# Performance work log

Hardware: AMD Instinct MI355X
Metric: run time of the kernel (lower is better)

The kernel has to match this reference:

```python
import jax, jax.numpy as jnp
import numpy as np

DIM = 1024
NUM_HEADS = 16
HEAD_DIM = DIM // NUM_HEADS
SCALE = HEAD_DIM ** -0.5


def setup_inputs() -> dict:
    key = jax.random.key(0)
    k_x, k_qw, k_qb, k_pw, k_pb = jax.random.split(key, 5)
    B, N = 4, 4096
    x = jax.random.normal(k_x, (B, N, DIM), dtype=jnp.float32)
    # nn.Linear(dim, 3*dim): weight (out, in), bias (out,)
    s = DIM ** -0.5
    qkv_w = jax.random.uniform(k_qw, (3 * DIM, DIM), jnp.float32, -s, s)
    qkv_b = jax.random.uniform(k_qb, (3 * DIM,), jnp.float32, -s, s)
    proj_w = jax.random.uniform(k_pw, (DIM, DIM), jnp.float32, -s, s)
    proj_b = jax.random.uniform(k_pb, (DIM,), jnp.float32, -s, s)
    return {"x": x, "qkv_w": qkv_w, "qkv_b": qkv_b,
            "proj_w": proj_w, "proj_b": proj_b}


def reference(x, qkv_w, qkv_b, proj_w, proj_b):
    B, N, C = x.shape
    H, D = NUM_HEADS, HEAD_DIM
    # qkv projection: (B,N,3C) -> (B,N,3,H,D)
    qkv = (jnp.einsum('bnc,oc->bno', x, qkv_w) + qkv_b).reshape(B, N, 3, H, D)
    q, k, v = qkv[:, :, 0], qkv[:, :, 1], qkv[:, :, 2]  # each (B,N,H,D)
    # Faithful to source: matmul over the last two dims of (B,N,H,D),
    # i.e. attention scores over the HEAD axis per token -> (B,N,H,H).
    attn = jnp.einsum('bnhd,bngd->bnhg', q, k) * SCALE
    attn = jax.nn.softmax(attn, axis=-1)
    out = jnp.einsum('bnhg,bngd->bnhd', attn, v)      # (B,N,H,D)
    # torch: .transpose(1,2).reshape(B,N,C) -> (B,H,N,D) reshaped to (B,N,C)
    out = out.transpose(0, 2, 1, 3).reshape(B, N, C)
    return jnp.einsum('bnc,oc->bno', out, proj_w) + proj_b
```

## Files before the change

kernel.cpp:

```cpp
#include <hip/hip_runtime.h>
#include <hip/hip_bf16.h>

#define TOK   16384
#define KD    1024
#define NQKV  3072
#define SEQL  4096
#define ATT_SCALE 0.125f

typedef __attribute__((ext_vector_type(4))) float f32x4;
typedef __attribute__((ext_vector_type(8))) short bf16x8;

__device__ __forceinline__ unsigned short f2b(float f){
    union { float f; unsigned u; } x; x.f = f;
    return (unsigned short)((x.u + 0x7FFFu + ((x.u >> 16) & 1u)) >> 16);
}
__device__ __forceinline__ float b2f(unsigned short s){
    union { unsigned u; float f; } x; x.u = ((unsigned)s) << 16;
    return x.f;
}
__device__ __forceinline__ bf16x8 lds8(const unsigned short* p){
    union { uint4 u; bf16x8 v; } t; t.u = *(const uint4*)p; return t.v;
}
__device__ __forceinline__ void glds16(const void* g, void* l){
    __builtin_amdgcn_global_load_lds((const __attribute__((address_space(1))) unsigned*)g,
                                     (__attribute__((address_space(3))) unsigned*)l, 16, 0, 0);
}

__global__ __launch_bounds__(256) void cvt_kernel(const float* __restrict__ in,
                                                  unsigned short* __restrict__ out, int n)
{
    int i = (blockIdx.x * 256 + threadIdx.x) * 8;
    if (i >= n) return;
    float4 a = *(const float4*)(in + i);
    float4 b = *(const float4*)(in + i + 4);
    union { unsigned short u[8]; uint4 v; } t;
    t.u[0]=f2b(a.x); t.u[1]=f2b(a.y); t.u[2]=f2b(a.z); t.u[3]=f2b(a.w);
    t.u[4]=f2b(b.x); t.u[5]=f2b(b.y); t.u[6]=f2b(b.z); t.u[7]=f2b(b.w);
    *(uint4*)(out + i) = t.v;
}

template<bool OUT_BF16>
__global__ __launch_bounds__(256) void gemm_kernel(const unsigned short* __restrict__ A,
        const unsigned short* __restrict__ Bw, const float* __restrict__ bias,
        void* __restrict__ Cp, int Nn)
{
    __shared__ unsigned short As[2][128 * 32];
    __shared__ unsigned short Bs[2][128 * 32];
    const int tid = threadIdx.x, lane = tid & 63;
    const int w = tid >> 6, wm = w >> 1, wn = w & 1;
    const int mBase = blockIdx.y * 128, cBase = blockIdx.x * 128;

    const int srow = w * 16 + (lane >> 2);
    const int sslot = (lane & 3) ^ ((lane >> 3) & 3);
    const unsigned short* Asrc = A  + (size_t)(mBase + srow) * KD + sslot * 8;
    const unsigned short* Bsrc = Bw + (size_t)(cBase + srow) * KD + sslot * 8;
    const int ldsOff = w * 512;

    f32x4 acc[4][4];
    #pragma unroll
    for (int m = 0; m < 4; m++)
        #pragma unroll
        for (int n = 0; n < 4; n++) acc[m][n] = (f32x4)0.f;

    const int rl = lane & 15;
    const int kslot = lane >> 4;
    const int rsw = (lane >> 1) & 3;

    #pragma unroll
    for (int j = 0; j < 2; j++) {
        glds16(Asrc + (size_t)j * 64 * KD, (void*)&As[0][j * 2048 + ldsOff]);
        glds16(Bsrc + (size_t)j * 64 * KD, (void*)&Bs[0][j * 2048 + ldsOff]);
    }

    int buf = 0;
    for (int kt = 0; kt < KD; kt += 32) {
        __syncthreads();
        if (kt + 32 < KD) {
            #pragma unroll
            for (int j = 0; j < 2; j++) {
                glds16(Asrc + (size_t)j * 64 * KD + kt + 32, (void*)&As[buf ^ 1][j * 2048 + ldsOff]);
                glds16(Bsrc + (size_t)j * 64 * KD + kt + 32, (void*)&Bs[buf ^ 1][j * 2048 + ldsOff]);
            }
        }
        bf16x8 af[4], bg[4];
        #pragma unroll
        for (int m = 0; m < 4; m++) {
            const int row = wm * 64 + m * 16 + rl;
            af[m] = lds8(&As[buf][row * 32 + ((kslot ^ rsw) * 8)]);
        }
        #pragma unroll
        for (int n = 0; n < 4; n++) {
            const int row = wn * 64 + n * 16 + rl;
            bg[n] = lds8(&Bs[buf][row * 32 + ((kslot ^ rsw) * 8)]);
        }
        #pragma unroll
        for (int m = 0; m < 4; m++)
            #pragma unroll
            for (int n = 0; n < 4; n++)
                acc[m][n] = __builtin_amdgcn_mfma_f32_16x16x32_bf16(af[m], bg[n], acc[m][n], 0, 0, 0);
        buf ^= 1;
    }

    #pragma unroll
    for (int n = 0; n < 4; n++) {
        const int col = cBase + wn * 64 + n * 16 + (lane & 15);
        const float bv = bias[col];
        #pragma unroll
        for (int m = 0; m < 4; m++) {
            const int row0 = mBase + wm * 64 + m * 16 + (lane >> 4) * 4;
            #pragma unroll
            for (int i = 0; i < 4; i++) {
                const float val = acc[m][n][i] + bv;
                if (OUT_BF16) ((unsigned short*)Cp)[(size_t)(row0 + i) * Nn + col] = f2b(val);
                else          ((float*)Cp)[(size_t)(row0 + i) * Nn + col] = val;
            }
        }
    }
}

__global__ __launch_bounds__(256) void attn_kernel(const unsigned short* __restrict__ qkv,
                                                   unsigned short* __restrict__ outp)
{
    __shared__ __align__(16) unsigned short qs[4][48 * 72];
    __shared__ float ps[4][16 * 17];
    const int tid = threadIdx.x, w = tid >> 6, lane = tid & 63;
    const int t = blockIdx.x * 4 + w;

    const unsigned short* src = qkv + (size_t)t * NQKV;
    #pragma unroll
    for (int i = 0; i < 6; i++) {
        const int e = i * 512 + lane * 8;
        uint4 v = *(const uint4*)(src + e);
        *(uint4*)&qs[w][(e >> 6) * 72 + (e & 63)] = v;
    }
    __syncthreads();

    const int h = lane & 15, g0 = lane >> 4;
    uint4 qv[8];
    #pragma unroll
    for (int i = 0; i < 8; i++) qv[i] = *(const uint4*)&qs[w][h * 72 + i * 8];
    float s[4];
    #pragma unroll
    for (int i = 0; i < 4; i++) {
        const int g = g0 * 4 + i;
        float a = 0.f;
        #pragma unroll
        for (int c = 0; c < 8; c++) {
            uint4 kv = *(const uint4*)&qs[w][(16 + g) * 72 + c * 8];
            uint qa[4] = {qv[c].x, qv[c].y, qv[c].z, qv[c].w};
            uint ka[4] = {kv.x, kv.y, kv.z, kv.w};
            #pragma unroll
            for (int u = 0; u < 4; u++) {
                a += b2f((unsigned short)qa[u]) * b2f((unsigned short)ka[u]);
                a += b2f((unsigned short)(qa[u] >> 16)) * b2f((unsigned short)(ka[u] >> 16));
            }
        }
        s[i] = a * ATT_SCALE;
    }
    float mx = fmaxf(fmaxf(s[0], s[1]), fmaxf(s[2], s[3]));
    mx = fmaxf(mx, __shfl_xor(mx, 16, 64));
    mx = fmaxf(mx, __shfl_xor(mx, 32, 64));
    float p[4], sm = 0.f;
    #pragma unroll
    for (int i = 0; i < 4; i++) { p[i] = __expf(s[i] - mx); sm += p[i]; }
    sm += __shfl_xor(sm, 16, 64);
    sm += __shfl_xor(sm, 32, 64);
    const float inv = 1.f / sm;
    #pragma unroll
    for (int i = 0; i < 4; i++) ps[w][h * 17 + g0 * 4 + i] = p[i] * inv;
    __syncthreads();

    const int h2 = lane >> 2, db = (lane & 3) * 16;
    float pr[16];
    #pragma unroll
    for (int g = 0; g < 16; g++) pr[g] = ps[w][h2 * 17 + g];
    float acc[16];
    #pragma unroll
    for (int j = 0; j < 16; j++) acc[j] = 0.f;
    #pragma unroll
    for (int g = 0; g < 16; g++) {
        const unsigned short* vp = &qs[w][(32 + g) * 72 + db];
        uint4 v0 = *(const uint4*)vp;
        uint4 v1 = *(const uint4*)(vp + 8);
        const float pg = pr[g];
        uint va[8] = {v0.x, v0.y, v0.z, v0.w, v1.x, v1.y, v1.z, v1.w};
        #pragma unroll
        for (int u = 0; u < 8; u++) {
            acc[2*u]   += pg * b2f((unsigned short)va[u]);
            acc[2*u+1] += pg * b2f((unsigned short)(va[u] >> 16));
        }
    }
    const int b = t >> 12, n = t & 4095;
    const int n1 = h2 * 256 + (n >> 4);
    const int c0 = (n & 15) * 64 + db;
    union { unsigned short u[16]; uint4 v[2]; } st;
    #pragma unroll
    for (int j = 0; j < 16; j++) st.u[j] = f2b(acc[j]);
    unsigned short* dst = outp + ((size_t)(b * SEQL + n1)) * 1024 + c0;
    *(uint4*)dst       = st.v[0];
    *(uint4*)(dst + 8) = st.v[1];
}

extern "C" void kernel_launch(void* const* d_in, const int* in_sizes, int n_in,
                              void* d_out, int out_size, void* d_ws, size_t ws_size,
                              hipStream_t stream)
{
    const float* x      = (const float*)d_in[0];
    const float* qkv_w  = (const float*)d_in[1];
    const float* qkv_b  = (const float*)d_in[2];
    const float* proj_w = (const float*)d_in[3];
    const float* proj_b = (const float*)d_in[4];

    unsigned short* xb  = (unsigned short*)d_ws;
    unsigned short* qkv = xb + (size_t)TOK * KD;
    unsigned short* qwb = qkv + (size_t)TOK * NQKV;
    unsigned short* pwb = qwb + (size_t)NQKV * KD;
    unsigned short* att = xb;

    cvt_kernel<<<dim3(TOK * KD / 2048), dim3(256), 0, stream>>>(x, xb, TOK * KD);
    cvt_kernel<<<dim3(NQKV * KD / 2048), dim3(256), 0, stream>>>(qkv_w, qwb, NQKV * KD);
    cvt_kernel<<<dim3(KD * KD / 2048), dim3(256), 0, stream>>>(proj_w, pwb, KD * KD);

    gemm_kernel<true><<<dim3(NQKV / 128, TOK / 128), dim3(256), 0, stream>>>(
        xb, qwb, qkv_b, qkv, NQKV);
    attn_kernel<<<dim3(TOK / 4), dim3(256), 0, stream>>>(qkv, att);
    gemm_kernel<false><<<dim3(KD / 128, TOK / 128), dim3(256), 0, stream>>>(
        att, pwb, proj_b, (float*)d_out, KD);
}
```

Measured before the change: 236.9 us.

## Replace 128x128 GEMM with 256x256 8-wave ping-pong pipelined kernel

Replaces the 128x128-tile, 4-wave GEMM with a 256x256-tile, 8-wave kernel that uses a BK of 64 and 128 KB of dynamic LDS. Inside each k-step, MFMA clusters are interleaved with staged global-to-LDS loads under explicit barriers and s_setprio. A workgroup-id remap spreads consecutive blocks across XCDs. The goal is higher arithmetic intensity and better overlap of loads with MFMA in both projections, at the cost of larger register and LDS use and many more barriers per k-step. The projection GEMM (N=1024) gets only 4 column tiles, so its grid is smaller.

```diff
diff --git a/kernel.cpp b/kernel.cpp
--- a/kernel.cpp
+++ b/kernel.cpp
@@ -40,74 +40,147 @@
 }
 
 template<bool OUT_BF16>
-__global__ __launch_bounds__(256) void gemm_kernel(const unsigned short* __restrict__ A,
+__global__ __launch_bounds__(512, 2) void gemm256(const unsigned short* __restrict__ A,
         const unsigned short* __restrict__ Bw, const float* __restrict__ bias,
         void* __restrict__ Cp, int Nn)
 {
-    __shared__ unsigned short As[2][128 * 32];
-    __shared__ unsigned short Bs[2][128 * 32];
+    extern __shared__ unsigned short sm[];
+    unsigned short* As = sm;
+    unsigned short* Bs = sm + 32768;
+
     const int tid = threadIdx.x, lane = tid & 63;
-    const int w = tid >> 6, wm = w >> 1, wn = w & 1;
-    const int mBase = blockIdx.y * 128, cBase = blockIdx.x * 128;
-
-    const int srow = w * 16 + (lane >> 2);
-    const int sslot = (lane & 3) ^ ((lane >> 3) & 3);
-    const unsigned short* Asrc = A  + (size_t)(mBase + srow) * KD + sslot * 8;
-    const unsigned short* Bsrc = Bw + (size_t)(cBase + srow) * KD + sslot * 8;
-    const int ldsOff = w * 512;
-
-    f32x4 acc[4][4];
-    #pragma unroll
-    for (int m = 0; m < 4; m++)
+    const int w = tid >> 6, wm = w >> 2, wn = w & 3;
+    const int rl = lane & 15, kslot = lane >> 4;
+
+    const int gx = gridDim.x;
+    const int nwg = gx * gridDim.y;
+    int id = blockIdx.y * gx + blockIdx.x;
+    id = (id & 7) * (nwg >> 3) + (id >> 3);
+    const int cBase = (id % gx) * 256;
+    const int mBase = (id / gx) * 256;
+
+    const int srcseg = ((tid & 7) ^ ((tid >> 3) & 7)) * 8;
+    const unsigned short* Ag = A  + (size_t)(mBase + (tid >> 3)) * KD + srcseg;
+    const unsigned short* Bg = Bw + (size_t)(cBase + (tid >> 3)) * KD + srcseg;
+
+    const int sA = (wm * 128 + rl) * 64;
+    const int sB = (wn * 64  + rl) * 64;
+    const int xk = rl & 7;
+    const int sk0 = (kslot ^ xk) * 8;
+    const int sk1 = ((4 + kslot) ^ xk) * 8;
+
+    f32x4 acc[8][4];
+    #pragma unroll
+    for (int m = 0; m < 8; m++)
         #pragma unroll
         for (int n = 0; n < 4; n++) acc[m][n] = (f32x4)0.f;
 
-    const int rl = lane & 15;
-    const int kslot = lane >> 4;
-    const int rsw = (lane >> 1) & 3;
-
-    #pragma unroll
-    for (int j = 0; j < 2; j++) {
-        glds16(Asrc + (size_t)j * 64 * KD, (void*)&As[0][j * 2048 + ldsOff]);
-        glds16(Bsrc + (size_t)j * 64 * KD, (void*)&Bs[0][j * 2048 + ldsOff]);
-    }
-
+#define STAGE_A(bb, kk) { \
+        glds16(Ag + (kk),          As + (bb)*16384 + tid*8); \
+        glds16(Ag + 64*KD + (kk),  As + (bb)*16384 + 4096  + tid*8); \
+        glds16(Ag + 128*KD + (kk), As + (bb)*16384 + 8192  + tid*8); \
+        glds16(Ag + 192*KD + (kk), As + (bb)*16384 + 12288 + tid*8); }
+#define STAGE_B(bb, kk) { \
+        glds16(Bg + (kk),          Bs + (bb)*16384 + tid*8); \
+        glds16(Bg + 64*KD + (kk),  Bs + (bb)*16384 + 4096  + tid*8); \
+        glds16(Bg + 128*KD + (kk), Bs + (bb)*16384 + 8192  + tid*8); \
+        glds16(Bg + 192*KD + (kk), Bs + (bb)*16384 + 12288 + tid*8); }
+
+    STAGE_A(0, 0)
+    STAGE_B(0, 0)
+    asm volatile("s_waitcnt vmcnt(0)" ::: "memory");
+    __builtin_amdgcn_s_barrier();
+
+    bf16x8 af[4][2], bfr[4][2];
     int buf = 0;
-    for (int kt = 0; kt < KD; kt += 32) {
-        __syncthreads();
-        if (kt + 32 < KD) {
-            #pragma unroll
-            for (int j = 0; j < 2; j++) {
-                glds16(Asrc + (size_t)j * 64 * KD + kt + 32, (void*)&As[buf ^ 1][j * 2048 + ldsOff]);
-                glds16(Bsrc + (size_t)j * 64 * KD + kt + 32, (void*)&Bs[buf ^ 1][j * 2048 + ldsOff]);
-            }
-        }
-        bf16x8 af[4], bg[4];
+    for (int kt = 0; kt < KD; kt += 64) {
+        const unsigned short* a = As + buf * 16384;
+        const unsigned short* b = Bs + buf * 16384;
+        const int nkt = kt + 64;
         #pragma unroll
         for (int m = 0; m < 4; m++) {
-            const int row = wm * 64 + m * 16 + rl;
-            af[m] = lds8(&As[buf][row * 32 + ((kslot ^ rsw) * 8)]);
-        }
-        #pragma unroll
-        for (int n = 0; n < 4; n++) {
-            const int row = wn * 64 + n * 16 + rl;
-            bg[n] = lds8(&Bs[buf][row * 32 + ((kslot ^ rsw) * 8)]);
-        }
+            af[m][0] = lds8(a + sA + m * 1024 + sk0);
+            af[m][1] = lds8(a + sA + m * 1024 + sk1);
+        }
+        #pragma unroll
+        for (int n = 0; n < 2; n++) {
+            bfr[n][0] = lds8(b + sB + n * 1024 + sk0);
+            bfr[n][1] = lds8(b + sB + n * 1024 + sk1);
+        }
+        if (nkt < KD) STAGE_A(buf ^ 1, nkt)
+        __builtin_amdgcn_s_barrier();
+        asm volatile("s_waitcnt lgkmcnt(0)" ::: "memory");
+        __builtin_amdgcn_sched_barrier(0);
+        __builtin_amdgcn_s_setprio(1);
         #pragma unroll
         for (int m = 0; m < 4; m++)
             #pragma unroll
-            for (int n = 0; n < 4; n++)
-                acc[m][n] = __builtin_amdgcn_mfma_f32_16x16x32_bf16(af[m], bg[n], acc[m][n], 0, 0, 0);
+            for (int n = 0; n < 2; n++) {
+                acc[m][n] = __builtin_amdgcn_mfma_f32_16x16x32_bf16(af[m][0], bfr[n][0], acc[m][n], 0, 0, 0);
+                acc[m][n] = __builtin_amdgcn_mfma_f32_16x16x32_bf16(af[m][1], bfr[n][1], acc[m][n], 0, 0, 0);
+            }
+        __builtin_amdgcn_s_setprio(0);
+        __builtin_amdgcn_s_barrier();
+        #pragma unroll
+        for (int n = 2; n < 4; n++) {
+            bfr[n][0] = lds8(b + sB + n * 1024 + sk0);
+            bfr[n][1] = lds8(b + sB + n * 1024 + sk1);
+        }
+        if (nkt < KD) STAGE_B(buf ^ 1, nkt)
+        __builtin_amdgcn_s_barrier();
+        asm volatile("s_waitcnt lgkmcnt(0)" ::: "memory");
+        __builtin_amdgcn_sched_barrier(0);
+        __builtin_amdgcn_s_setprio(1);
+        #pragma unroll
+        for (int m = 0; m < 4; m++)
+            #pragma unroll
+            for (int n = 2; n < 4; n++) {
+                acc[m][n] = __builtin_amdgcn_mfma_f32_16x16x32_bf16(af[m][0], bfr[n][0], acc[m][n], 0, 0, 0);
+                acc[m][n] = __builtin_amdgcn_mfma_f32_16x16x32_bf16(af[m][1], bfr[n][1], acc[m][n], 0, 0, 0);
+            }
+        __builtin_amdgcn_s_setprio(0);
+        __builtin_amdgcn_s_barrier();
+        #pragma unroll
+        for (int m = 0; m < 4; m++) {
+            af[m][0] = lds8(a + sA + (m + 4) * 1024 + sk0);
+            af[m][1] = lds8(a + sA + (m + 4) * 1024 + sk1);
+        }
+        __builtin_amdgcn_s_barrier();
+        asm volatile("s_waitcnt lgkmcnt(0)" ::: "memory");
+        __builtin_amdgcn_sched_barrier(0);
+        __builtin_amdgcn_s_setprio(1);
+        #pragma unroll
+        for (int m = 0; m < 4; m++)
+            #pragma unroll
+            for (int n = 0; n < 2; n++) {
+                acc[4 + m][n] = __builtin_amdgcn_mfma_f32_16x16x32_bf16(af[m][0], bfr[n][0], acc[4 + m][n], 0, 0, 0);
+                acc[4 + m][n] = __builtin_amdgcn_mfma_f32_16x16x32_bf16(af[m][1], bfr[n][1], acc[4 + m][n], 0, 0, 0);
+            }
+        __builtin_amdgcn_s_setprio(0);
+        __builtin_amdgcn_s_barrier();
+        __builtin_amdgcn_s_setprio(1);
+        #pragma unroll
+        for (int m = 0; m < 4; m++)
+            #pragma unroll
+            for (int n = 2; n < 4; n++) {
+                acc[4 + m][n] = __builtin_amdgcn_mfma_f32_16x16x32_bf16(af[m][0], bfr[n][0], acc[4 + m][n], 0, 0, 0);
+                acc[4 + m][n] = __builtin_amdgcn_mfma_f32_16x16x32_bf16(af[m][1], bfr[n][1], acc[4 + m][n], 0, 0, 0);
+            }
+        __builtin_amdgcn_s_setprio(0);
+        asm volatile("s_waitcnt vmcnt(0)" ::: "memory");
+        __builtin_amdgcn_s_barrier();
         buf ^= 1;
     }
+#undef STAGE_A
+#undef STAGE_B
 
     #pragma unroll
     for (int n = 0; n < 4; n++) {
-        const int col = cBase + wn * 64 + n * 16 + (lane & 15);
+        const int col = cBase + wn * 64 + n * 16 + rl;
         const float bv = bias[col];
         #pragma unroll
-        for (int m = 0; m < 4; m++) {
-            const int row0 = mBase + wm * 64 + m * 16 + (lane >> 4) * 4;
+        for (int m = 0; m < 8; m++) {
+            const int row0 = mBase + wm * 128 + m * 16 + kslot * 4;
             #pragma unroll
             for (int i = 0; i < 4; i++) {
                 const float val = acc[m][n][i] + bv;
@@ -160,12 +233,12 @@
     float mx = fmaxf(fmaxf(s[0], s[1]), fmaxf(s[2], s[3]));
     mx = fmaxf(mx, __shfl_xor(mx, 16, 64));
     mx = fmaxf(mx, __shfl_xor(mx, 32, 64));
-    float p[4], sm = 0.f;
-    #pragma unroll
-    for (int i = 0; i < 4; i++) { p[i] = __expf(s[i] - mx); sm += p[i]; }
-    sm += __shfl_xor(sm, 16, 64);
-    sm += __shfl_xor(sm, 32, 64);
-    const float inv = 1.f / sm;
+    float p[4], smv = 0.f;
+    #pragma unroll
+    for (int i = 0; i < 4; i++) { p[i] = __expf(s[i] - mx); smv += p[i]; }
+    smv += __shfl_xor(smv, 16, 64);
+    smv += __shfl_xor(smv, 32, 64);
+    const float inv = 1.f / smv;
     #pragma unroll
     for (int i = 0; i < 4; i++) ps[w][h * 17 + g0 * 4 + i] = p[i] * inv;
     __syncthreads();
@@ -217,13 +290,18 @@
     unsigned short* pwb = qwb + (size_t)NQKV * KD;
     unsigned short* att = xb;
 
+    hipFuncSetAttribute(reinterpret_cast<const void*>(&gemm256<true>),
+                        hipFuncAttributeMaxDynamicSharedMemorySize, 131072);
+    hipFuncSetAttribute(reinterpret_cast<const void*>(&gemm256<false>),
+                        hipFuncAttributeMaxDynamicSharedMemorySize, 131072);
+
     cvt_kernel<<<dim3(TOK * KD / 2048), dim3(256), 0, stream>>>(x, xb, TOK * KD);
     cvt_kernel<<<dim3(NQKV * KD / 2048), dim3(256), 0, stream>>>(qkv_w, qwb, NQKV * KD);
     cvt_kernel<<<dim3(KD * KD / 2048), dim3(256), 0, stream>>>(proj_w, pwb, KD * KD);
 
-    gemm_kernel<true><<<dim3(NQKV / 128, TOK / 128), dim3(256), 0, stream>>>(
+    gemm256<true><<<dim3(NQKV / 256, TOK / 256), dim3(512), 131072, stream>>>(
         xb, qwb, qkv_b, qkv, NQKV);
     attn_kernel<<<dim3(TOK / 4), dim3(256), 0, stream>>>(qkv, att);
-    gemm_kernel<false><<<dim3(KD / 128, TOK / 128), dim3(256), 0, stream>>>(
+    gemm256<false><<<dim3(KD / 256, TOK / 256), dim3(512), 131072, stream>>>(
         att, pwb, proj_b, (float*)d_out, KD);
 }
```

New measurement: 215.6 us. 9.0% less time.
